# Kernel tuning notes

Measured on AMD Instinct MI355X. Metric: run time of the kernel, lower is better.

## Reference

```python
import jax, jax.numpy as jnp
import numpy as np

B = 2048; SQ = 64; PC = 24; F = 16; H = 128; D = 256; T = 128; A = 4672
NSQ = B * SQ; NPC = B * PC


def setup_inputs() -> dict:
    key = jax.random.key(0)
    ks = iter(jax.random.split(key, 48))
    def nrm(shape, s=0.05):
        return jax.random.normal(next(ks), shape, dtype=jnp.float32) * s
    def edges(e_per, src_per, dst_per):
        # per-graph local edges: graph_offset + local node index
        g = jnp.repeat(jnp.arange(B), e_per)
        src = g * src_per + jax.random.randint(next(ks), (B * e_per,), 0, src_per)
        dst = g * dst_per + jax.random.randint(next(ks), (B * e_per,), 0, dst_per)
        return jnp.stack([src, dst]).astype(jnp.int32)
    gp = jnp.repeat(jnp.arange(B), PC)
    occ_src = jnp.arange(NPC, dtype=jnp.int32)                       # each piece occupies one square
    occ_dst = (gp * SQ + jax.random.randint(next(ks), (NPC,), 0, SQ)).astype(jnp.int32)
    ei_occ = jnp.stack([occ_src, occ_dst])                           # piece -> square
    ei_rev = ei_occ[::-1]                                            # square -> piece (rev_occupied_by)
    return dict(
        x_sq=jax.random.normal(next(ks), (NSQ, F), dtype=jnp.float32),
        x_pc=jax.random.normal(next(ks), (NPC, F), dtype=jnp.float32),
        W_in_sq=nrm((F, H)), b_in_sq=jnp.zeros((H,), jnp.float32),
        W_in_pc=nrm((F, H)), b_in_pc=jnp.zeros((H,), jnp.float32),
        W_adj=nrm((H, H)), W_occ=nrm((H, H)), W_att=nrm((H, H)), W_def=nrm((H, H)), W_rev=nrm((H, H)),
        W_out=nrm((H, D)), b_out=jnp.zeros((D,), jnp.float32),
        W_pt=nrm((D, T)), b_pt=jnp.zeros((T,), jnp.float32),
        W_vt=nrm((D, T)), b_vt=jnp.zeros((T,), jnp.float32),
        W_ph=nrm((T, A)), b_ph=jnp.zeros((A,), jnp.float32),
        W_vh=nrm((T, 1)), b_vh=jnp.zeros((1,), jnp.float32),
        ei_adj=edges(420, SQ, SQ),
        ei_occ=ei_occ,
        ei_att=edges(40, PC, PC),
        ei_def=edges(40, PC, PC),
        ei_rev=ei_rev,
        square_batch=jnp.repeat(jnp.arange(B), SQ).astype(jnp.int32),
        piece_batch=gp.astype(jnp.int32),
    )


def reference(x_sq, x_pc, W_in_sq, b_in_sq, W_in_pc, b_in_pc,
              W_adj, W_occ, W_att, W_def, W_rev, W_out, b_out,
              W_pt, b_pt, W_vt, b_vt, W_ph, b_ph, W_vh, b_vh,
              ei_adj, ei_occ, ei_att, ei_def, ei_rev, square_batch, piece_batch):
    gelu = jax.nn.gelu
    seg = jax.ops.segment_sum
    # per-node-type input encoders
    h_sq = gelu(x_sq @ W_in_sq + b_in_sq)          # [NSQ, H]
    h_pc = gelu(x_pc @ W_in_pc + b_in_pc)          # [NPC, H]
    # heterogeneous message passing: gather -> linear -> scatter-sum per edge type
    agg_sq = seg(h_sq[ei_adj[0]] @ W_adj, ei_adj[1], NSQ)
    agg_sq = agg_sq + seg(h_pc[ei_occ[0]] @ W_occ, ei_occ[1], NSQ)
    agg_pc = seg(h_pc[ei_att[0]] @ W_att, ei_att[1], NPC)
    agg_pc = agg_pc + seg(h_pc[ei_def[0]] @ W_def, ei_def[1], NPC)
    agg_pc = agg_pc + seg(h_sq[ei_rev[0]] @ W_rev, ei_rev[1], NPC)
    h_sq2 = gelu(h_sq + agg_sq)
    h_pc2 = gelu(h_pc + agg_pc)
    # project to embed_dim and mean-pool per graph
    out_sq = gelu(h_sq2 @ W_out + b_out)           # [NSQ, D]
    out_pc = gelu(h_pc2 @ W_out + b_out)           # [NPC, D]
    shared = seg(out_sq, square_batch, B) / SQ + seg(out_pc, piece_batch, B) / PC  # [B, D]
    # dual trunks + heads (exactly as in ChessNetwork.forward)
    policy_logits = gelu(shared @ W_pt + b_pt) @ W_ph + b_ph        # [B, 4672]
    value = jnp.tanh(gelu(shared @ W_vt + b_vt) @ W_vh + b_vh)      # [B, 1]
    return policy_logits, value
```

## Files before the change

kernel.cpp:

```cpp
#include <hip/hip_runtime.h>

#define BATCH 2048
#define SQN 64
#define PCN 24
#define FEAT 16
#define HID 128
#define DOUT 256
#define TDIM 128
#define ADIM 4672
#define NSQT (BATCH*SQN)
#define NPCT (BATCH*PCN)
#define E_ADJ 420
#define E_ATT 40
#define E_ADJ_TOT (BATCH*E_ADJ)
#define E_ATT_TOT (BATCH*E_ATT)

typedef unsigned short u16;
typedef unsigned int u32;
typedef __attribute__((ext_vector_type(8))) short bf16x8;
typedef __attribute__((ext_vector_type(8))) unsigned short u16x8;
typedef __attribute__((ext_vector_type(4))) float f32x4;

#define OFF_WADJ_H 0
#define OFF_WADJ_L 16384
#define OFF_WOCC_H 32768
#define OFF_WOCC_L 49152
#define OFF_WATT_H 65536
#define OFF_WATT_L 81920
#define OFF_WDEF_H 98304
#define OFF_WDEF_L 114688
#define OFF_WREV_H 131072
#define OFF_WREV_L 147456
#define OFF_WOUT_H 163840
#define OFF_WOUT_L 196608
#define OFF_WPH_H  229376
#define OFF_WPH_L  827392
#define OFF_WINSQ_H 1425408
#define OFF_WINSQ_L 1429504
#define OFF_WINPC_H 1433600
#define OFF_WINPC_L 1437696
#define WB_TOTAL    1441792

#define HS_OFF   0
#define AH_OFF   32768
#define AL_OFF   49152
#define HP_OFF   65536
#define EPK_OFF  71680
#define SRT_OFF  73360
#define RSA_OFF  75040
#define CURA_OFF 75300
#define CNTA_OFF 75556
#define RSO_OFF  75812
#define CURO_OFF 76072
#define CNTO_OFF 76328
#define SRTO_OFF 76584
#define OPK_OFF  76680
#define KSQ_SMEM 76776

#define PHP_OFF  0
#define PAH_OFF  24576
#define PAL_OFF  36864
#define PEA_OFF  49152
#define PED_OFF  49472
#define PSA_OFF  49792
#define PSD_OFF  50112
#define PRSA_OFF 50432
#define PCUA_OFF 50692
#define PCNA_OFF 50948
#define PRSD_OFF 51204
#define PCUD_OFF 51464
#define PCND_OFF 51720
#define PRVS_OFF 51976
#define PRVD_OFF 52168

__device__ __forceinline__ float gelu_f(float x) {
    float z = 0.7978845608028654f * (x + 0.044715f * x * x * x);
    float e = __expf(2.0f * z);
    float t = 1.0f - 2.0f / (e + 1.0f);
    return 0.5f * x * (1.0f + t);
}
__device__ __forceinline__ u16 f2b(float x) {
    u32 u = __float_as_uint(x);
    u += 0x7fffu + ((u >> 16) & 1u);
    return (u16)(u >> 16);
}
__device__ __forceinline__ float b2f(u16 h) { return __uint_as_float(((u32)h) << 16); }
__device__ __forceinline__ void split2(float x, u16& h, u16& l) {
    u16 hh = f2b(x); h = hh; l = f2b(x - b2f(hh));
}
__device__ __forceinline__ f32x4 MFMA(bf16x8 a, bf16x8 b, f32x4 c) {
    return __builtin_amdgcn_mfma_f32_16x16x32_bf16(a, b, c, 0, 0, 0);
}
__device__ __forceinline__ bf16x8 bzero() {
    bf16x8 v = {0,0,0,0,0,0,0,0}; return v;
}
__device__ __forceinline__ void xfrag(const float* __restrict__ xrow, int g,
                                      bf16x8& ah, bf16x8& al)
{
    f32x4 a = *(const f32x4*)(xrow + g*8);
    f32x4 b = *(const f32x4*)(xrow + g*8 + 4);
    #pragma unroll
    for (int j = 0; j < 4; ++j) {
        u16 h, l;
        split2(a[j], h, l); ah[j]   = (short)h; al[j]   = (short)l;
        split2(b[j], h, l); ah[4+j] = (short)h; al[4+j] = (short)l;
    }
}

template<int NT, int RT>
__device__ __forceinline__ void gemm_nt(
    const unsigned char* Ah, const unsigned char* Al,
    const u16* __restrict__ wh, const u16* __restrict__ wl,
    int ntBase, int lane, int g, int lr, f32x4 (&c)[NT][RT])
{
    const int sw = lr << 4;
    #pragma unroll
    for (int ks = 0; ks < 4; ++ks) {
        const int ko = ks*64 + g*16;
        bf16x8 ah[RT], al[RT];
        #pragma unroll
        for (int rt = 0; rt < RT; ++rt) {
            const int ro = (rt*16 + lr)*256 + (ko ^ sw);
            ah[rt] = *(const bf16x8*)(Ah + ro);
            al[rt] = *(const bf16x8*)(Al + ro);
        }
        #pragma unroll
        for (int ntl = 0; ntl < NT; ++ntl) {
            bf16x8 bh = *(const bf16x8*)(wh + (((ntBase+ntl)*4 + ks)*64 + lane)*8);
            bf16x8 bl = *(const bf16x8*)(wl + (((ntBase+ntl)*4 + ks)*64 + lane)*8);
            #pragma unroll
            for (int rt = 0; rt < RT; ++rt) {
                c[ntl][rt] = MFMA(ah[rt], bh, c[ntl][rt]);
                c[ntl][rt] = MFMA(al[rt], bh, c[ntl][rt]);
                c[ntl][rt] = MFMA(ah[rt], bl, c[ntl][rt]);
            }
        }
    }
}

__device__ __forceinline__ void gather_f32_8(
    const unsigned char* H, const int* srt, int st, int en, int cq8, float (&acc)[16])
{
    for (int i = st; i < en; ++i) {
        const int s = srt[i];
        const unsigned char* rp = H + s*512;
        const int sw2 = (s & 15) << 4;
        #pragma unroll
        for (int u = 0; u < 4; ++u) {
            f32x4 v = *(const f32x4*)(rp + ((cq8*64 + u*16) ^ sw2));
            acc[u*4+0] += v[0]; acc[u*4+1] += v[1];
            acc[u*4+2] += v[2]; acc[u*4+3] += v[3];
        }
    }
}
__device__ __forceinline__ void gather_b16_8(
    const unsigned char* H, const int* srt, int st, int en, int cq8, float (&acc)[16])
{
    for (int i = st; i < en; ++i) {
        const int s = srt[i];
        const unsigned char* rp = H + s*256;
        const int sw2 = (s & 15) << 4;
        #pragma unroll
        for (int u = 0; u < 2; ++u) {
            u16x8 v = *(const u16x8*)(rp + ((cq8*32 + u*16) ^ sw2));
            #pragma unroll
            for (int j = 0; j < 8; ++j) acc[u*8+j] += b2f(v[j]);
        }
    }
}
__device__ __forceinline__ void writeA_8(
    unsigned char* Ah, unsigned char* Al, int d, int cq8, const float (&acc)[16])
{
    unsigned char* wh = Ah + d*256;
    unsigned char* wl = Al + d*256;
    const int dw = (d & 15) << 4;
    #pragma unroll
    for (int u = 0; u < 2; ++u) {
        u16x8 oh, ol;
        #pragma unroll
        for (int j = 0; j < 8; ++j) {
            float x = acc[u*8+j];
            u16 h = f2b(x); oh[j] = h; ol[j] = f2b(x - b2f(h));
        }
        *(u16x8*)(wh + ((cq8*32 + u*16) ^ dw)) = oh;
        *(u16x8*)(wl + ((cq8*32 + u*16) ^ dw)) = ol;
    }
}

__global__ __launch_bounds__(256) void k_prep(
    const float* __restrict__ W_adj, const float* __restrict__ W_occ,
    const float* __restrict__ W_att, const float* __restrict__ W_def,
    const float* __restrict__ W_rev, const float* __restrict__ W_out,
    const float* __restrict__ W_ph,
    const float* __restrict__ W_in_sq, const float* __restrict__ W_in_pc,
    u16* __restrict__ wb)
{
    int gid = blockIdx.x*256 + threadIdx.x;
    int fid = gid >> 6, lane = gid & 63;
    int g8 = (lane >> 4) * 8, lr = lane & 15;
    u16x8 vh, vl;
    if (fid >= 1392) {
        int f = fid - 1392;
        const float* src = (f < 8) ? W_in_sq : W_in_pc;
        int oh = (f < 8) ? OFF_WINSQ_H : OFF_WINPC_H;
        int ol = (f < 8) ? OFF_WINSQ_L : OFF_WINPC_L;
        int nt = f & 7;
        int col = nt*16 + lr;
        #pragma unroll
        for (int j = 0; j < 8; ++j) {
            int k = g8 + j;
            float v = (k < 16) ? src[k*HID + col] : 0.f;
            u16 h, l; split2(v, h, l);
            vh[j] = h; vl[j] = l;
        }
        *(u16x8*)(wb + oh + (nt*64 + lane)*8) = vh;
        *(u16x8*)(wb + ol + (nt*64 + lane)*8) = vl;
        return;
    }
    const float* src; int ld, f, oh, ol;
    if (fid < 32)       { src = W_adj; ld = HID;  f = fid;      oh = OFF_WADJ_H; ol = OFF_WADJ_L; }
    else if (fid < 64)  { src = W_occ; ld = HID;  f = fid-32;   oh = OFF_WOCC_H; ol = OFF_WOCC_L; }
    else if (fid < 96)  { src = W_att; ld = HID;  f = fid-64;   oh = OFF_WATT_H; ol = OFF_WATT_L; }
    else if (fid < 128) { src = W_def; ld = HID;  f = fid-96;   oh = OFF_WDEF_H; ol = OFF_WDEF_L; }
    else if (fid < 160) { src = W_rev; ld = HID;  f = fid-128;  oh = OFF_WREV_H; ol = OFF_WREV_L; }
    else if (fid < 224) { src = W_out; ld = DOUT; f = fid-160;  oh = OFF_WOUT_H; ol = OFF_WOUT_L; }
    else                { src = W_ph;  ld = ADIM; f = fid-224;  oh = OFF_WPH_H;  ol = OFF_WPH_L; }
    int nt = f >> 2, kb = f & 3;
    int col = nt*16 + lr;
    #pragma unroll
    for (int j = 0; j < 8; ++j) {
        int k = kb*32 + g8 + j;
        u16 h, l; split2(src[k*ld + col], h, l);
        vh[j] = h; vl[j] = l;
    }
    *(u16x8*)(wb + oh + (f*64 + lane)*8) = vh;
    *(u16x8*)(wb + ol + (f*64 + lane)*8) = vl;
}

__device__ __forceinline__ void sq_path(
    unsigned char* SMb, int b, int t,
    const float* __restrict__ x_sq, const float* __restrict__ x_pc,
    const float* __restrict__ b_in_sq, const float* __restrict__ b_in_pc,
    const float* __restrict__ b_out,
    const int* __restrict__ ei_adj, const int* __restrict__ ei_occ,
    const u16* __restrict__ wb, float* __restrict__ shared_sq)
{
    unsigned char* Hs = SMb + HS_OFF;
    unsigned char* Ah = SMb + AH_OFF;
    unsigned char* Al = SMb + AL_OFF;
    unsigned char* Hp = SMb + HP_OFF;
    int* e_pk  = (int*)(SMb + EPK_OFF);
    int* srt_a = (int*)(SMb + SRT_OFF);
    int* rs_a  = (int*)(SMb + RSA_OFF);
    int* cur_a = (int*)(SMb + CURA_OFF);
    int* cnt_a = (int*)(SMb + CNTA_OFF);
    int* rs_o  = (int*)(SMb + RSO_OFF);
    int* cur_o = (int*)(SMb + CURO_OFF);
    int* cnt_o = (int*)(SMb + CNTO_OFF);
    int* srt_o = (int*)(SMb + SRTO_OFF);
    int* o_pk  = (int*)(SMb + OPK_OFF);

    const int w = t >> 6, lane = t & 63, g = lane >> 4, lr = lane & 15;

    for (int i = t; i < E_ADJ; i += 512) {
        int s = ei_adj[b*E_ADJ + i] - b*SQN;
        int d = ei_adj[E_ADJ_TOT + b*E_ADJ + i] - b*SQN;
        e_pk[i] = s | (d << 16);
    }
    if (t < PCN) {
        int s = ei_occ[b*PCN + t] - b*PCN;
        int d = ei_occ[NPCT + b*PCN + t] - b*SQN;
        o_pk[t] = s | (d << 16);
    }
    if (t < 64) { cnt_a[t] = 0; cnt_o[t] = 0; }
    __syncthreads();

    for (int i = t; i < E_ADJ; i += 512) atomicAdd(&cnt_a[e_pk[i] >> 16], 1);
    if (t < PCN) atomicAdd(&cnt_o[o_pk[t] >> 16], 1);
    __syncthreads();

    if (t < 64) {
        int v = cnt_a[t], o0 = v;
        for (int o = 1; o < 64; o <<= 1) { int u = __shfl_up(v, o); if (t >= o) v += u; }
        rs_a[t+1] = v; cur_a[t] = v - o0; if (t == 0) rs_a[0] = 0;
    } else if (t < 128) {
        int l = t - 64;
        int v = cnt_o[l], o0 = v;
        for (int o = 1; o < 64; o <<= 1) { int u = __shfl_up(v, o); if (l >= o) v += u; }
        rs_o[l+1] = v; cur_o[l] = v - o0; if (l == 0) rs_o[0] = 0;
    }
    __syncthreads();

    for (int i = t; i < E_ADJ; i += 512) {
        int pk = e_pk[i];
        int p = atomicAdd(&cur_a[pk >> 16], 1);
        srt_a[p] = pk & 0xffff;
    }
    if (t < PCN) {
        int pk = o_pk[t];
        int p = atomicAdd(&cur_o[pk >> 16], 1);
        srt_o[p] = pk & 0xffff;
    }
    {
        const int colp = w*16 + lr;
        f32x4 ch[4];
        const f32x4 z = {0.f,0.f,0.f,0.f};
        #pragma unroll
        for (int rt = 0; rt < 4; ++rt) ch[rt] = z;
        {
            bf16x8 bh = *(const bf16x8*)(wb + OFF_WINSQ_H + (w*64 + lane)*8);
            bf16x8 bl = *(const bf16x8*)(wb + OFF_WINSQ_L + (w*64 + lane)*8);
            #pragma unroll
            for (int rt = 0; rt < 4; ++rt) {
                bf16x8 ah = bzero(), al = bzero();
                if (g < 2) xfrag(x_sq + (b*SQN + rt*16 + lr)*FEAT, g, ah, al);
                ch[rt] = MFMA(ah, bh, ch[rt]);
                ch[rt] = MFMA(al, bh, ch[rt]);
                ch[rt] = MFMA(ah, bl, ch[rt]);
            }
        }
        const float bbs = b_in_sq[colp];
        #pragma unroll
        for (int rt = 0; rt < 4; ++rt)
            #pragma unroll
            for (int r = 0; r < 4; ++r) {
                const int row = rt*16 + g*4 + r;
                float h = gelu_f(ch[rt][r] + bbs);
                *(float*)(Hs + row*512 + ((colp*4) ^ ((row&15)<<4))) = h;
            }
        f32x4 cp[2];
        cp[0] = z; cp[1] = z;
        {
            bf16x8 bh = *(const bf16x8*)(wb + OFF_WINPC_H + (w*64 + lane)*8);
            bf16x8 bl = *(const bf16x8*)(wb + OFF_WINPC_L + (w*64 + lane)*8);
            #pragma unroll
            for (int rt = 0; rt < 2; ++rt) {
                const int row = rt*16 + lr;
                bf16x8 ah = bzero(), al = bzero();
                if (g < 2 && row < PCN) xfrag(x_pc + (b*PCN + row)*FEAT, g, ah, al);
                cp[rt] = MFMA(ah, bh, cp[rt]);
                cp[rt] = MFMA(al, bh, cp[rt]);
                cp[rt] = MFMA(ah, bl, cp[rt]);
            }
        }
        const float bbp = b_in_pc[colp];
        #pragma unroll
        for (int rt = 0; rt < 2; ++rt)
            #pragma unroll
            for (int r = 0; r < 4; ++r) {
                const int row = rt*16 + g*4 + r;
                if (row < PCN) {
                    float h = gelu_f(cp[rt][r] + bbp);
                    *(u16*)(Hp + row*256 + ((colp*2) ^ ((row&15)<<4))) = f2b(h);
                }
            }
    }
    __syncthreads();

    {
        const int d = t >> 3, cq8 = t & 7;
        float acc[16];
        #pragma unroll
        for (int i = 0; i < 16; ++i) acc[i] = 0.f;
        gather_f32_8(Hs, srt_a, rs_a[d], rs_a[d+1], cq8, acc);
        writeA_8(Ah, Al, d, cq8, acc);
    }
    __syncthreads();

    f32x4 c1[1][4];
    {
        const f32x4 z = {0.f,0.f,0.f,0.f};
        #pragma unroll
        for (int rt = 0; rt < 4; ++rt) c1[0][rt] = z;
    }
    gemm_nt<1,4>(Ah, Al, wb + OFF_WADJ_H, wb + OFF_WADJ_L, w, lane, g, lr, c1);
    __syncthreads();

    {
        const int d = t >> 3, cq8 = t & 7;
        float acc[16];
        #pragma unroll
        for (int i = 0; i < 16; ++i) acc[i] = 0.f;
        gather_b16_8(Hp, srt_o, rs_o[d], rs_o[d+1], cq8, acc);
        writeA_8(Ah, Al, d, cq8, acc);
    }
    __syncthreads();

    gemm_nt<1,4>(Ah, Al, wb + OFF_WOCC_H, wb + OFF_WOCC_L, w, lane, g, lr, c1);
    __syncthreads();

    {
        const int colp = w*16 + lr;
        #pragma unroll
        for (int rt = 0; rt < 4; ++rt)
            #pragma unroll
            for (int r = 0; r < 4; ++r) {
                const int row = rt*16 + g*4 + r;
                float hv = *(const float*)(Hs + row*512 + ((colp*4) ^ ((row&15)<<4)));
                float h2 = gelu_f(c1[0][rt][r] + hv);
                u16 hh, ll; split2(h2, hh, ll);
                const int bo = row*256 + ((colp*2) ^ ((row&15)<<4));
                *(u16*)(Ah + bo) = hh;
                *(u16*)(Al + bo) = ll;
            }
    }
    __syncthreads();

    f32x4 c2[2][4];
    {
        const f32x4 z = {0.f,0.f,0.f,0.f};
        #pragma unroll
        for (int n = 0; n < 2; ++n)
            #pragma unroll
            for (int rt = 0; rt < 4; ++rt) c2[n][rt] = z;
    }
    gemm_nt<2,4>(Ah, Al, wb + OFF_WOUT_H, wb + OFF_WOUT_L, w*2, lane, g, lr, c2);
    #pragma unroll
    for (int ntl = 0; ntl < 2; ++ntl) {
        const int col = (w*2 + ntl)*16 + lr;
        const float bias = b_out[col];
        float cs = 0.f;
        #pragma unroll
        for (int rt = 0; rt < 4; ++rt)
            #pragma unroll
            for (int r = 0; r < 4; ++r) cs += gelu_f(c2[ntl][rt][r] + bias);
        cs += __shfl_xor(cs, 16);
        cs += __shfl_xor(cs, 32);
        if (lane < 16) shared_sq[b*DOUT + col] = cs * (1.0f/64.0f);
    }
}

__device__ __forceinline__ void pc_path(
    unsigned char* SMb, int pcb, int t,
    const float* __restrict__ x_sq, const float* __restrict__ x_pc,
    const float* __restrict__ b_in_sq, const float* __restrict__ b_in_pc,
    const float* __restrict__ b_out,
    const int* __restrict__ ei_att, const int* __restrict__ ei_def,
    const int* __restrict__ ei_rev,
    const u16* __restrict__ wb, float* __restrict__ shared_pc)
{
    unsigned char* Hp = SMb + PHP_OFF;
    unsigned char* Ah = SMb + PAH_OFF;
    unsigned char* Al = SMb + PAL_OFF;
    int* ea_pk = (int*)(SMb + PEA_OFF);
    int* ed_pk = (int*)(SMb + PED_OFF);
    int* srt_a = (int*)(SMb + PSA_OFF);
    int* srt_d = (int*)(SMb + PSD_OFF);
    int* rs_a  = (int*)(SMb + PRSA_OFF);
    int* cur_a = (int*)(SMb + PCUA_OFF);
    int* cnt_a = (int*)(SMb + PCNA_OFF);
    int* rs_d  = (int*)(SMb + PRSD_OFF);
    int* cur_d = (int*)(SMb + PCUD_OFF);
    int* cnt_d = (int*)(SMb + PCND_OFF);
    int* rv_s  = (int*)(SMb + PRVS_OFF);
    int* rv_d  = (int*)(SMb + PRVD_OFF);

    const int w = t >> 6, lane = t & 63, g = lane >> 4, lr = lane & 15;
    const int NR = 2*PCN;

    for (int i = t; i < 2*E_ATT; i += 512) {
        int sb = (i >= E_ATT) ? 1 : 0;
        int e = i - sb*E_ATT;
        int gb = pcb*2 + sb;
        int ro = sb*PCN - gb*PCN;
        int s = ei_att[gb*E_ATT + e] + ro;
        int d = ei_att[E_ATT_TOT + gb*E_ATT + e] + ro;
        ea_pk[i] = s | (d << 16);
        s = ei_def[gb*E_ATT + e] + ro;
        d = ei_def[E_ATT_TOT + gb*E_ATT + e] + ro;
        ed_pk[i] = s | (d << 16);
    }
    if (t < NR) {
        int sb = (t >= PCN) ? 1 : 0;
        int gb = pcb*2 + sb;
        int p = t - sb*PCN;
        rv_s[t] = ei_rev[gb*PCN + p];
        rv_d[t] = ei_rev[NPCT + gb*PCN + p] - gb*PCN + sb*PCN;
    }
    if (t < 64) { cnt_a[t] = 0; cnt_d[t] = 0; }
    __syncthreads();

    for (int i = t; i < 2*E_ATT; i += 512) {
        atomicAdd(&cnt_a[ea_pk[i] >> 16], 1);
        atomicAdd(&cnt_d[ed_pk[i] >> 16], 1);
    }
    __syncthreads();

    if (t < 64) {
        int v = cnt_a[t], o0 = v;
        for (int o = 1; o < 64; o <<= 1) { int u = __shfl_up(v, o); if (t >= o) v += u; }
        rs_a[t+1] = v; cur_a[t] = v - o0; if (t == 0) rs_a[0] = 0;
    } else if (t < 128) {
        int l = t - 64;
        int v = cnt_d[l], o0 = v;
        for (int o = 1; o < 64; o <<= 1) { int u = __shfl_up(v, o); if (l >= o) v += u; }
        rs_d[l+1] = v; cur_d[l] = v - o0; if (l == 0) rs_d[0] = 0;
    }
    __syncthreads();

    for (int i = t; i < 2*E_ATT; i += 512) {
        int pk = ea_pk[i];
        int p = atomicAdd(&cur_a[pk >> 16], 1); srt_a[p] = pk & 0xffff;
        pk = ed_pk[i];
        p = atomicAdd(&cur_d[pk >> 16], 1); srt_d[p] = pk & 0xffff;
    }
    {
        const int colp = w*16 + lr;
        const f32x4 z = {0.f,0.f,0.f,0.f};
        f32x4 cp[3];
        #pragma unroll
        for (int rt = 0; rt < 3; ++rt) cp[rt] = z;
        {
            bf16x8 bh = *(const bf16x8*)(wb + OFF_WINPC_H + (w*64 + lane)*8);
            bf16x8 bl = *(const bf16x8*)(wb + OFF_WINPC_L + (w*64 + lane)*8);
            #pragma unroll
            for (int rt = 0; rt < 3; ++rt) {
                bf16x8 ah = bzero(), al = bzero();
                if (g < 2) xfrag(x_pc + (pcb*NR + rt*16 + lr)*FEAT, g, ah, al);
                cp[rt] = MFMA(ah, bh, cp[rt]);
                cp[rt] = MFMA(al, bh, cp[rt]);
                cp[rt] = MFMA(ah, bl, cp[rt]);
            }
        }
        const float bbp = b_in_pc[colp];
        #pragma unroll
        for (int rt = 0; rt < 3; ++rt)
            #pragma unroll
            for (int r = 0; r < 4; ++r) {
                const int row = rt*16 + g*4 + r;
                float h = gelu_f(cp[rt][r] + bbp);
                *(float*)(Hp + row*512 + ((colp*4) ^ ((row&15)<<4))) = h;
            }
        f32x4 cr[3];
        #pragma unroll
        for (int rt = 0; rt < 3; ++rt) cr[rt] = z;
        {
            bf16x8 bh = *(const bf16x8*)(wb + OFF_WINSQ_H + (w*64 + lane)*8);
            bf16x8 bl = *(const bf16x8*)(wb + OFF_WINSQ_L + (w*64 + lane)*8);
            #pragma unroll
            for (int rt = 0; rt < 3; ++rt) {
                bf16x8 ah = bzero(), al = bzero();
                if (g < 2) {
                    int gr = rv_s[rt*16 + lr];
                    xfrag(x_sq + gr*FEAT, g, ah, al);
                }
                cr[rt] = MFMA(ah, bh, cr[rt]);
                cr[rt] = MFMA(al, bh, cr[rt]);
                cr[rt] = MFMA(ah, bl, cr[rt]);
            }
        }
        const float bbs = b_in_sq[colp];
        #pragma unroll
        for (int rt = 0; rt < 3; ++rt)
            #pragma unroll
            for (int r = 0; r < 4; ++r) {
                const int row0 = rt*16 + g*4 + r;
                const int dr = rv_d[row0];
                float h = gelu_f(cr[rt][r] + bbs);
                u16 hh, ll; split2(h, hh, ll);
                const int bo = dr*256 + ((colp*2) ^ ((dr&15)<<4));
                *(u16*)(Ah + bo) = hh;
                *(u16*)(Al + bo) = ll;
            }
    }
    __syncthreads();

    f32x4 c1[1][3];
    {
        const f32x4 z = {0.f,0.f,0.f,0.f};
        #pragma unroll
        for (int rt = 0; rt < 3; ++rt) c1[0][rt] = z;
    }
    gemm_nt<1,3>(Ah, Al, wb + OFF_WREV_H, wb + OFF_WREV_L, w, lane, g, lr, c1);
    __syncthreads();

    {
        const int d = t >> 3, cq8 = t & 7;
        if (d < NR) {
            float acc[16];
            #pragma unroll
            for (int i = 0; i < 16; ++i) acc[i] = 0.f;
            gather_f32_8(Hp, srt_a, rs_a[d], rs_a[d+1], cq8, acc);
            writeA_8(Ah, Al, d, cq8, acc);
        }
    }
    __syncthreads();

    gemm_nt<1,3>(Ah, Al, wb + OFF_WATT_H, wb + OFF_WATT_L, w, lane, g, lr, c1);
    __syncthreads();

    {
        const int d = t >> 3, cq8 = t & 7;
        if (d < NR) {
            float acc[16];
            #pragma unroll
            for (int i = 0; i < 16; ++i) acc[i] = 0.f;
            gather_f32_8(Hp, srt_d, rs_d[d], rs_d[d+1], cq8, acc);
            writeA_8(Ah, Al, d, cq8, acc);
        }
    }
    __syncthreads();

    gemm_nt<1,3>(Ah, Al, wb + OFF_WDEF_H, wb + OFF_WDEF_L, w, lane, g, lr, c1);
    __syncthreads();

    {
        const int colp = w*16 + lr;
        #pragma unroll
        for (int rt = 0; rt < 3; ++rt)
            #pragma unroll
            for (int r = 0; r < 4; ++r) {
                const int row = rt*16 + g*4 + r;
                float hv = *(const float*)(Hp + row*512 + ((colp*4) ^ ((row&15)<<4)));
                float h2 = gelu_f(c1[0][rt][r] + hv);
                u16 hh, ll; split2(h2, hh, ll);
                const int bo = row*256 + ((colp*2) ^ ((row&15)<<4));
                *(u16*)(Ah + bo) = hh;
                *(u16*)(Al + bo) = ll;
            }
    }
    __syncthreads();

    f32x4 c2[2][3];
    {
        const f32x4 z = {0.f,0.f,0.f,0.f};
        #pragma unroll
        for (int n = 0; n < 2; ++n)
            #pragma unroll
            for (int rt = 0; rt < 3; ++rt) c2[n][rt] = z;
    }
    gemm_nt<2,3>(Ah, Al, wb + OFF_WOUT_H, wb + OFF_WOUT_L, w*2, lane, g, lr, c2);
    #pragma unroll
    for (int ntl = 0; ntl < 2; ++ntl) {
        const int col = (w*2 + ntl)*16 + lr;
        const float bias = b_out[col];
        float s0 = 0.f, s1 = 0.f;
        #pragma unroll
        for (int r = 0; r < 4; ++r) s0 += gelu_f(c2[ntl][0][r] + bias);
        {
            float tt = 0.f;
            #pragma unroll
            for (int r = 0; r < 4; ++r) tt += gelu_f(c2[ntl][1][r] + bias);
            s0 += (g < 2) ? tt : 0.f;
            s1 += (g < 2) ? 0.f : tt;
        }
        #pragma unroll
        for (int r = 0; r < 4; ++r) s1 += gelu_f(c2[ntl][2][r] + bias);
        s0 += __shfl_xor(s0, 16); s0 += __shfl_xor(s0, 32);
        s1 += __shfl_xor(s1, 16); s1 += __shfl_xor(s1, 32);
        if (lane < 16) {
            const int b0 = pcb*2, b1 = b0 + 1;
            shared_pc[b0*DOUT + col] = s0 * (1.0f/PCN);
            shared_pc[b1*DOUT + col] = s1 * (1.0f/PCN);
        }
    }
}

__global__ __launch_bounds__(512, 4) void k_main(
    const float* __restrict__ x_sq, const float* __restrict__ x_pc,
    const float* __restrict__ b_in_sq, const float* __restrict__ b_in_pc,
    const float* __restrict__ b_out,
    const int* __restrict__ ei_adj, const int* __restrict__ ei_occ,
    const int* __restrict__ ei_att, const int* __restrict__ ei_def,
    const int* __restrict__ ei_rev,
    const u16* __restrict__ wb,
    float* __restrict__ shared_sq, float* __restrict__ shared_pc)
{
    extern __shared__ __align__(16) unsigned char SMb[];
    const int bid = blockIdx.x;
    const int grp = bid / 3, rem = bid - grp*3;
    if (rem < 2) {
        sq_path(SMb, grp*2 + rem, threadIdx.x, x_sq, x_pc, b_in_sq, b_in_pc,
                b_out, ei_adj, ei_occ, wb, shared_sq);
    } else {
        pc_path(SMb, grp, threadIdx.x, x_sq, x_pc, b_in_sq, b_in_pc,
                b_out, ei_att, ei_def, ei_rev, wb, shared_pc);
    }
}

__global__ __launch_bounds__(256) void k_head(
    const float* __restrict__ shared_sq, const float* __restrict__ shared_pc,
    const float* __restrict__ W_pt, const float* __restrict__ b_pt,
    const float* __restrict__ W_vt, const float* __restrict__ b_vt,
    const float* __restrict__ W_vh, const float* __restrict__ b_vh,
    u16* __restrict__ tpol_h, u16* __restrict__ tpol_l, float* __restrict__ out_value)
{
    __shared__ float sh[2*DOUT];
    __shared__ float vred[2*TDIM];
    const int t = threadIdx.x;
    const int hh = t >> 7, j = t & 127;
    const int b = blockIdx.x*2 + hh;
    for (int i = t; i < 2*DOUT; i += 256)
        sh[i] = shared_sq[blockIdx.x*2*DOUT + i] + shared_pc[blockIdx.x*2*DOUT + i];
    __syncthreads();
    const float* s = sh + hh*DOUT;
    float ap = b_pt[j], av = b_vt[j];
    #pragma unroll 8
    for (int k = 0; k < DOUT; ++k) {
        float sv = s[k];
        ap += sv * W_pt[k*TDIM + j];
        av += sv * W_vt[k*TDIM + j];
    }
    float tv = gelu_f(ap);
    u16 th, tl; split2(tv, th, tl);
    tpol_h[b*TDIM + j] = th;
    tpol_l[b*TDIM + j] = tl;
    vred[hh*TDIM + j] = gelu_f(av) * W_vh[j];
    __syncthreads();
    for (int stp = 64; stp > 0; stp >>= 1) {
        if (j < stp) vred[hh*TDIM + j] += vred[hh*TDIM + j + stp];
        __syncthreads();
    }
    if (j == 0) out_value[b] = tanhf(vred[hh*TDIM] + b_vh[0]);
}

__global__ __launch_bounds__(256) void k_pol(
    const u16* __restrict__ tpol_h, const u16* __restrict__ tpol_l,
    const u16* __restrict__ wb, const float* __restrict__ b_ph,
    float* __restrict__ pol)
{
    const u16* wph_h = wb + OFF_WPH_H;
    const u16* wph_l = wb + OFF_WPH_L;
    const int t = threadIdx.x, w = t >> 6, lane = t & 63, g = lane >> 4, lr = lane & 15;
    const int nt = blockIdx.x*4 + w;
    const int rbase = blockIdx.y*64;
    f32x4 acc[4];
    const f32x4 z = {0.f,0.f,0.f,0.f};
    #pragma unroll
    for (int rt = 0; rt < 4; ++rt) acc[rt] = z;
    #pragma unroll
    for (int ks = 0; ks < 4; ++ks) {
        bf16x8 bh = *(const bf16x8*)(wph_h + ((nt*4 + ks)*64 + lane)*8);
        bf16x8 bl = *(const bf16x8*)(wph_l + ((nt*4 + ks)*64 + lane)*8);
        #pragma unroll
        for (int rt = 0; rt < 4; ++rt) {
            const int ro = (rbase + rt*16 + lr)*TDIM + ks*32 + g*8;
            bf16x8 ah = *(const bf16x8*)(tpol_h + ro);
            bf16x8 al = *(const bf16x8*)(tpol_l + ro);
            acc[rt] = MFMA(ah, bh, acc[rt]);
            acc[rt] = MFMA(al, bh, acc[rt]);
            acc[rt] = MFMA(ah, bl, acc[rt]);
        }
    }
    const float bias = b_ph[nt*16 + lr];
    #pragma unroll
    for (int rt = 0; rt < 4; ++rt)
        #pragma unroll
        for (int r = 0; r < 4; ++r) {
            int row = rbase + rt*16 + g*4 + r;
            pol[(size_t)row*ADIM + nt*16 + lr] = acc[rt][r] + bias;
        }
}

extern "C" void kernel_launch(void* const* d_in, const int* in_sizes, int n_in,
                              void* d_out, int out_size, void* d_ws, size_t ws_size,
                              hipStream_t stream) {
    (void)in_sizes; (void)n_in; (void)out_size; (void)ws_size;
    const float* x_sq    = (const float*)d_in[0];
    const float* x_pc    = (const float*)d_in[1];
    const float* W_in_sq = (const float*)d_in[2];
    const float* b_in_sq = (const float*)d_in[3];
    const float* W_in_pc = (const float*)d_in[4];
    const float* b_in_pc = (const float*)d_in[5];
    const float* W_adj   = (const float*)d_in[6];
    const float* W_occ   = (const float*)d_in[7];
    const float* W_att   = (const float*)d_in[8];
    const float* W_def   = (const float*)d_in[9];
    const float* W_rev   = (const float*)d_in[10];
    const float* W_out   = (const float*)d_in[11];
    const float* b_out   = (const float*)d_in[12];
    const float* W_pt    = (const float*)d_in[13];
    const float* b_pt    = (const float*)d_in[14];
    const float* W_vt    = (const float*)d_in[15];
    const float* b_vt    = (const float*)d_in[16];
    const float* W_ph    = (const float*)d_in[17];
    const float* b_ph    = (const float*)d_in[18];
    const float* W_vh    = (const float*)d_in[19];
    const float* b_vh    = (const float*)d_in[20];
    const int* ei_adj    = (const int*)d_in[21];
    const int* ei_occ    = (const int*)d_in[22];
    const int* ei_att    = (const int*)d_in[23];
    const int* ei_def    = (const int*)d_in[24];
    const int* ei_rev    = (const int*)d_in[25];

    float* out = (float*)d_out;
    float* pol = out;
    float* val = out + (size_t)BATCH * ADIM;

    float* shared_sq = (float*)d_ws;
    float* shared_pc = shared_sq + BATCH*DOUT;
    u16* tpol_h = (u16*)(shared_pc + BATCH*DOUT);
    u16* tpol_l = tpol_h + BATCH*TDIM;
    u16* wb     = tpol_l + BATCH*TDIM;

    hipFuncSetAttribute((const void*)k_main,
                        hipFuncAttributeMaxDynamicSharedMemorySize, KSQ_SMEM);

    k_prep<<<352, 256, 0, stream>>>(W_adj, W_occ, W_att, W_def, W_rev, W_out, W_ph,
                                    W_in_sq, W_in_pc, wb);
    k_main<<<3072, 512, KSQ_SMEM, stream>>>(x_sq, x_pc, b_in_sq, b_in_pc, b_out,
                                            ei_adj, ei_occ, ei_att, ei_def, ei_rev,
                                            wb, shared_sq, shared_pc);
    k_head<<<BATCH/2, 256, 0, stream>>>(shared_sq, shared_pc, W_pt, b_pt, W_vt, b_vt,
                                        W_vh, b_vh, tpol_h, tpol_l, val);
    k_pol<<<dim3(ADIM/64, BATCH/64), 256, 0, stream>>>(tpol_h, tpol_l, wb, b_ph, pol);
}
```

Baseline: 226.8 us.

## Replace square-path CSR gather with dense adjacency-matrix MFMA and reorder linear before aggregation

The square path no longer sorts edges into CSR and gathers rows. It builds a dense 64x64 edge-count matrix and a 64x24 occupancy matrix in shared memory, multiplies H by W_adj and W_occ first, then aggregates with MFMA against those matrices. GELU is rewritten into a cheaper algebraic form, and bf16 splitting now uses the packed v_cvt_pk_bf16_f32 instruction. Edge counts stored as bf16 are exact only while they stay small, and shared memory use grows to 80 KB, which may reduce occupancy.

```diff
diff --git a/kernel.cpp b/kernel.cpp
--- a/kernel.cpp
+++ b/kernel.cpp
@@ -20,6 +20,8 @@
 typedef __attribute__((ext_vector_type(8))) short bf16x8;
 typedef __attribute__((ext_vector_type(8))) unsigned short u16x8;
 typedef __attribute__((ext_vector_type(4))) float f32x4;
+typedef __attribute__((ext_vector_type(2))) unsigned int u32x2;
+typedef __attribute__((ext_vector_type(4))) unsigned int u32x4;
 
 #define OFF_WADJ_H 0
 #define OFF_WADJ_L 16384
@@ -41,21 +43,7 @@
 #define OFF_WINPC_L 1437696
 #define WB_TOTAL    1441792
 
-#define HS_OFF   0
-#define AH_OFF   32768
-#define AL_OFF   49152
-#define HP_OFF   65536
-#define EPK_OFF  71680
-#define SRT_OFF  73360
-#define RSA_OFF  75040
-#define CURA_OFF 75300
-#define CNTA_OFF 75556
-#define RSO_OFF  75812
-#define CURO_OFF 76072
-#define CNTO_OFF 76328
-#define SRTO_OFF 76584
-#define OPK_OFF  76680
-#define KSQ_SMEM 76776
+#define K_SMEM 81920
 
 #define PHP_OFF  0
 #define PAH_OFF  24576
@@ -73,20 +61,30 @@
 #define PRVS_OFF 51976
 #define PRVD_OFF 52168
 
-__device__ __forceinline__ float gelu_f(float x) {
-    float z = 0.7978845608028654f * (x + 0.044715f * x * x * x);
-    float e = __expf(2.0f * z);
-    float t = 1.0f - 2.0f / (e + 1.0f);
-    return 0.5f * x * (1.0f + t);
-}
-__device__ __forceinline__ u16 f2b(float x) {
-    u32 u = __float_as_uint(x);
-    u += 0x7fffu + ((u >> 16) & 1u);
-    return (u16)(u >> 16);
-}
+__device__ __forceinline__ u32 cvtpk(float a, float b) {
+    u32 r;
+    asm("v_cvt_pk_bf16_f32 %0, %1, %2" : "=v"(r) : "v"(a), "v"(b));
+    return r;
+}
+__device__ __forceinline__ u16 f2b(float x) { return (u16)cvtpk(x, x); }
 __device__ __forceinline__ float b2f(u16 h) { return __uint_as_float(((u32)h) << 16); }
 __device__ __forceinline__ void split2(float x, u16& h, u16& l) {
-    u16 hh = f2b(x); h = hh; l = f2b(x - b2f(hh));
+    u32 wp = cvtpk(x, x);
+    h = (u16)wp;
+    float r = x - __uint_as_float(wp << 16);
+    l = (u16)cvtpk(r, r);
+}
+__device__ __forceinline__ void split_pk(float a, float b, u32& wh, u32& wl) {
+    wh = cvtpk(a, b);
+    float ra = a - __uint_as_float(wh << 16);
+    float rb = b - __uint_as_float(wh & 0xffff0000u);
+    wl = cvtpk(ra, rb);
+}
+__device__ __forceinline__ float gelu_f(float x) {
+    float x2 = x * x;
+    float z2 = x * __builtin_fmaf(x2, 0.0713548162f, 1.5957691216f);
+    float e = __expf(z2);
+    return x - x * __fdividef(1.0f, e + 1.0f);
 }
 __device__ __forceinline__ f32x4 MFMA(bf16x8 a, bf16x8 b, f32x4 c) {
     return __builtin_amdgcn_mfma_f32_16x16x32_bf16(a, b, c, 0, 0, 0);
@@ -97,14 +95,17 @@
 __device__ __forceinline__ void xfrag(const float* __restrict__ xrow, int g,
                                       bf16x8& ah, bf16x8& al)
 {
-    f32x4 a = *(const f32x4*)(xrow + g*8);
-    f32x4 b = *(const f32x4*)(xrow + g*8 + 4);
-    #pragma unroll
-    for (int j = 0; j < 4; ++j) {
-        u16 h, l;
-        split2(a[j], h, l); ah[j]   = (short)h; al[j]   = (short)l;
-        split2(b[j], h, l); ah[4+j] = (short)h; al[4+j] = (short)l;
-    }
+    const f32x4 a = *(const f32x4*)(xrow + g*8);
+    const f32x4 b = *(const f32x4*)(xrow + g*8 + 4);
+    u32 h0,h1,h2,h3,l0,l1,l2,l3;
+    split_pk(a[0], a[1], h0, l0);
+    split_pk(a[2], a[3], h1, l1);
+    split_pk(b[0], b[1], h2, l2);
+    split_pk(b[2], b[3], h3, l3);
+    u32x4 vh = {h0,h1,h2,h3};
+    u32x4 vl = {l0,l1,l2,l3};
+    ah = *(bf16x8*)&vh;
+    al = *(bf16x8*)&vl;
 }
 
 template<int NT, int RT>
@@ -153,21 +154,6 @@
         }
     }
 }
-__device__ __forceinline__ void gather_b16_8(
-    const unsigned char* H, const int* srt, int st, int en, int cq8, float (&acc)[16])
-{
-    for (int i = st; i < en; ++i) {
-        const int s = srt[i];
-        const unsigned char* rp = H + s*256;
-        const int sw2 = (s & 15) << 4;
-        #pragma unroll
-        for (int u = 0; u < 2; ++u) {
-            u16x8 v = *(const u16x8*)(rp + ((cq8*32 + u*16) ^ sw2));
-            #pragma unroll
-            for (int j = 0; j < 8; ++j) acc[u*8+j] += b2f(v[j]);
-        }
-    }
-}
 __device__ __forceinline__ void writeA_8(
     unsigned char* Ah, unsigned char* Al, int d, int cq8, const float (&acc)[16])
 {
@@ -176,14 +162,14 @@
     const int dw = (d & 15) << 4;
     #pragma unroll
     for (int u = 0; u < 2; ++u) {
-        u16x8 oh, ol;
-        #pragma unroll
-        for (int j = 0; j < 8; ++j) {
-            float x = acc[u*8+j];
-            u16 h = f2b(x); oh[j] = h; ol[j] = f2b(x - b2f(h));
-        }
-        *(u16x8*)(wh + ((cq8*32 + u*16) ^ dw)) = oh;
-        *(u16x8*)(wl + ((cq8*32 + u*16) ^ dw)) = ol;
+        u32 oh[4], ol[4];
+        #pragma unroll
+        for (int j = 0; j < 4; ++j)
+            split_pk(acc[u*8 + j*2], acc[u*8 + j*2 + 1], oh[j], ol[j]);
+        u32x4 vh = {oh[0], oh[1], oh[2], oh[3]};
+        u32x4 vl = {ol[0], ol[1], ol[2], ol[3]};
+        *(u32x4*)(wh + ((cq8*32 + u*16) ^ dw)) = vh;
+        *(u32x4*)(wl + ((cq8*32 + u*16) ^ dw)) = vl;
     }
 }
 
@@ -245,68 +231,51 @@
     const int* __restrict__ ei_adj, const int* __restrict__ ei_occ,
     const u16* __restrict__ wb, float* __restrict__ shared_sq)
 {
-    unsigned char* Hs = SMb + HS_OFF;
-    unsigned char* Ah = SMb + AH_OFF;
-    unsigned char* Al = SMb + AL_OFF;
-    unsigned char* Hp = SMb + HP_OFF;
-    int* e_pk  = (int*)(SMb + EPK_OFF);
-    int* srt_a = (int*)(SMb + SRT_OFF);
-    int* rs_a  = (int*)(SMb + RSA_OFF);
-    int* cur_a = (int*)(SMb + CURA_OFF);
-    int* cnt_a = (int*)(SMb + CNTA_OFF);
-    int* rs_o  = (int*)(SMb + RSO_OFF);
-    int* cur_o = (int*)(SMb + CURO_OFF);
-    int* cnt_o = (int*)(SMb + CNTO_OFF);
-    int* srt_o = (int*)(SMb + SRTO_OFF);
-    int* o_pk  = (int*)(SMb + OPK_OFF);
+    unsigned char* Hs_h  = SMb;
+    unsigned char* Hs_l  = SMb + 16384;
+    int*           Mint  = (int*)(SMb + 32768);
+    unsigned char* HOT_h = SMb + 32768;
+    unsigned char* HOT_l = SMb + 40960;
+    unsigned char* Mocc  = SMb + 49152;
+    unsigned char* A_h   = SMb + 32768;
+    unsigned char* A_l   = SMb + 49152;
+    unsigned char* Madj  = SMb + 65536;
+    unsigned char* Hp    = SMb + 73728;
 
     const int w = t >> 6, lane = t & 63, g = lane >> 4, lr = lane & 15;
+    const int colp = w*16 + lr;
+
+    #pragma unroll
+    for (int i = 0; i < 8; ++i) Mint[t + i*512] = 0;
+    ((u32*)Mocc)[t] = 0;
+    ((u32*)Mocc)[t + 512] = 0;
+    ((u32*)(Hp + 6144))[t] = 0;
+    __syncthreads();
 
     for (int i = t; i < E_ADJ; i += 512) {
         int s = ei_adj[b*E_ADJ + i] - b*SQN;
         int d = ei_adj[E_ADJ_TOT + b*E_ADJ + i] - b*SQN;
-        e_pk[i] = s | (d << 16);
+        atomicAdd(&Mint[d*64 + s], 1);
     }
     if (t < PCN) {
-        int s = ei_occ[b*PCN + t] - b*PCN;
+        int p = ei_occ[b*PCN + t] - b*PCN;
         int d = ei_occ[NPCT + b*PCN + t] - b*SQN;
-        o_pk[t] = s | (d << 16);
-    }
-    if (t < 64) { cnt_a[t] = 0; cnt_o[t] = 0; }
-    __syncthreads();
-
-    for (int i = t; i < E_ADJ; i += 512) atomicAdd(&cnt_a[e_pk[i] >> 16], 1);
-    if (t < PCN) atomicAdd(&cnt_o[o_pk[t] >> 16], 1);
-    __syncthreads();
-
-    if (t < 64) {
-        int v = cnt_a[t], o0 = v;
-        for (int o = 1; o < 64; o <<= 1) { int u = __shfl_up(v, o); if (t >= o) v += u; }
-        rs_a[t+1] = v; cur_a[t] = v - o0; if (t == 0) rs_a[0] = 0;
-    } else if (t < 128) {
-        int l = t - 64;
-        int v = cnt_o[l], o0 = v;
-        for (int o = 1; o < 64; o <<= 1) { int u = __shfl_up(v, o); if (l >= o) v += u; }
-        rs_o[l+1] = v; cur_o[l] = v - o0; if (l == 0) rs_o[0] = 0;
-    }
-    __syncthreads();
-
-    for (int i = t; i < E_ADJ; i += 512) {
-        int pk = e_pk[i];
-        int p = atomicAdd(&cur_a[pk >> 16], 1);
-        srt_a[p] = pk & 0xffff;
-    }
-    if (t < PCN) {
-        int pk = o_pk[t];
-        int p = atomicAdd(&cur_o[pk >> 16], 1);
-        srt_o[p] = pk & 0xffff;
-    }
-    {
-        const int colp = w*16 + lr;
-        f32x4 ch[4];
+        *(u16*)(Mocc + d*64 + ((p*2) ^ ((d&3)<<4))) = 0x3F80;
+    }
+    __syncthreads();
+
+    #pragma unroll
+    for (int ii = 0; ii < 4; ++ii) {
+        int i = t + ii*512;
+        int row = i >> 5, cp = i & 31;
+        float v0 = (float)Mint[row*64 + cp*2];
+        float v1 = (float)Mint[row*64 + cp*2 + 1];
+        *(u32*)(Madj + row*128 + ((cp*4) ^ ((row&7)<<4))) = cvtpk(v0, v1);
+    }
+    float hv[16];
+    {
         const f32x4 z = {0.f,0.f,0.f,0.f};
-        #pragma unroll
-        for (int rt = 0; rt < 4; ++rt) ch[rt] = z;
+        f32x4 ch[4] = {z,z,z,z};
         {
             bf16x8 bh = *(const bf16x8*)(wb + OFF_WINSQ_H + (w*64 + lane)*8);
             bf16x8 bl = *(const bf16x8*)(wb + OFF_WINSQ_L + (w*64 + lane)*8);
@@ -326,10 +295,13 @@
             for (int r = 0; r < 4; ++r) {
                 const int row = rt*16 + g*4 + r;
                 float h = gelu_f(ch[rt][r] + bbs);
-                *(float*)(Hs + row*512 + ((colp*4) ^ ((row&15)<<4))) = h;
-            }
-        f32x4 cp[2];
-        cp[0] = z; cp[1] = z;
+                hv[rt*4 + r] = h;
+                u16 hh, ll; split2(h, hh, ll);
+                const int bo = row*256 + ((colp*2) ^ ((row&15)<<4));
+                *(u16*)(Hs_h + bo) = hh;
+                *(u16*)(Hs_l + bo) = ll;
+            }
+        f32x4 cp2[2] = {z, z};
         {
             bf16x8 bh = *(const bf16x8*)(wb + OFF_WINPC_H + (w*64 + lane)*8);
             bf16x8 bl = *(const bf16x8*)(wb + OFF_WINPC_L + (w*64 + lane)*8);
@@ -338,9 +310,9 @@
                 const int row = rt*16 + lr;
                 bf16x8 ah = bzero(), al = bzero();
                 if (g < 2 && row < PCN) xfrag(x_pc + (b*PCN + row)*FEAT, g, ah, al);
-                cp[rt] = MFMA(ah, bh, cp[rt]);
-                cp[rt] = MFMA(al, bh, cp[rt]);
-                cp[rt] = MFMA(ah, bl, cp[rt]);
+                cp2[rt] = MFMA(ah, bh, cp2[rt]);
+                cp2[rt] = MFMA(al, bh, cp2[rt]);
+                cp2[rt] = MFMA(ah, bl, cp2[rt]);
             }
         }
         const float bbp = b_in_pc[colp];
@@ -350,60 +322,114 @@
             for (int r = 0; r < 4; ++r) {
                 const int row = rt*16 + g*4 + r;
                 if (row < PCN) {
-                    float h = gelu_f(cp[rt][r] + bbp);
+                    float h = gelu_f(cp2[rt][r] + bbp);
                     *(u16*)(Hp + row*256 + ((colp*2) ^ ((row&15)<<4))) = f2b(h);
                 }
             }
     }
     __syncthreads();
 
-    {
-        const int d = t >> 3, cq8 = t & 7;
-        float acc[16];
-        #pragma unroll
-        for (int i = 0; i < 16; ++i) acc[i] = 0.f;
-        gather_f32_8(Hs, srt_a, rs_a[d], rs_a[d+1], cq8, acc);
-        writeA_8(Ah, Al, d, cq8, acc);
-    }
-    __syncthreads();
-
-    f32x4 c1[1][4];
+    f32x4 hwj[4], hwo[2];
     {
         const f32x4 z = {0.f,0.f,0.f,0.f};
-        #pragma unroll
-        for (int rt = 0; rt < 4; ++rt) c1[0][rt] = z;
-    }
-    gemm_nt<1,4>(Ah, Al, wb + OFF_WADJ_H, wb + OFF_WADJ_L, w, lane, g, lr, c1);
-    __syncthreads();
-
-    {
-        const int d = t >> 3, cq8 = t & 7;
-        float acc[16];
-        #pragma unroll
-        for (int i = 0; i < 16; ++i) acc[i] = 0.f;
-        gather_b16_8(Hp, srt_o, rs_o[d], rs_o[d+1], cq8, acc);
-        writeA_8(Ah, Al, d, cq8, acc);
-    }
-    __syncthreads();
-
-    gemm_nt<1,4>(Ah, Al, wb + OFF_WOCC_H, wb + OFF_WOCC_L, w, lane, g, lr, c1);
-    __syncthreads();
-
-    {
-        const int colp = w*16 + lr;
-        #pragma unroll
-        for (int rt = 0; rt < 4; ++rt)
-            #pragma unroll
-            for (int r = 0; r < 4; ++r) {
-                const int row = rt*16 + g*4 + r;
-                float hv = *(const float*)(Hs + row*512 + ((colp*4) ^ ((row&15)<<4)));
-                float h2 = gelu_f(c1[0][rt][r] + hv);
-                u16 hh, ll; split2(h2, hh, ll);
-                const int bo = row*256 + ((colp*2) ^ ((row&15)<<4));
-                *(u16*)(Ah + bo) = hh;
-                *(u16*)(Al + bo) = ll;
-            }
-    }
+        hwj[0]=z; hwj[1]=z; hwj[2]=z; hwj[3]=z; hwo[0]=z; hwo[1]=z;
+        const int sw15 = lr << 4;
+        #pragma unroll
+        for (int ks = 0; ks < 4; ++ks) {
+            const int ko = ks*64 + g*16;
+            bf16x8 bh = *(const bf16x8*)(wb + OFF_WADJ_H + ((w*4 + ks)*64 + lane)*8);
+            bf16x8 bl = *(const bf16x8*)(wb + OFF_WADJ_L + ((w*4 + ks)*64 + lane)*8);
+            #pragma unroll
+            for (int rt = 0; rt < 4; ++rt) {
+                const int ro = (rt*16 + lr)*256 + (ko ^ sw15);
+                bf16x8 ah = *(const bf16x8*)(Hs_h + ro);
+                bf16x8 al = *(const bf16x8*)(Hs_l + ro);
+                hwj[rt] = MFMA(ah, bh, hwj[rt]);
+                hwj[rt] = MFMA(al, bh, hwj[rt]);
+                hwj[rt] = MFMA(ah, bl, hwj[rt]);
+            }
+            bf16x8 oh = *(const bf16x8*)(wb + OFF_WOCC_H + ((w*4 + ks)*64 + lane)*8);
+            bf16x8 ol = *(const bf16x8*)(wb + OFF_WOCC_L + ((w*4 + ks)*64 + lane)*8);
+            #pragma unroll
+            for (int rt = 0; rt < 2; ++rt) {
+                const int ro = (rt*16 + lr)*256 + (ko ^ sw15);
+                bf16x8 ah = *(const bf16x8*)(Hp + ro);
+                hwo[rt] = MFMA(ah, oh, hwo[rt]);
+                hwo[rt] = MFMA(ah, ol, hwo[rt]);
+            }
+        }
+    }
+    __syncthreads();
+
+    {
+        const int swj = (lr & 7) << 4;
+        #pragma unroll
+        for (int rt = 0; rt < 4; ++rt) {
+            u32 h01, l01, h23, l23;
+            split_pk(hwj[rt][0], hwj[rt][1], h01, l01);
+            split_pk(hwj[rt][2], hwj[rt][3], h23, l23);
+            const int off = colp*128 + ((rt*32 + g*8) ^ swj);
+            *(u32x2*)(Hs_h + off) = (u32x2){h01, h23};
+            *(u32x2*)(Hs_l + off) = (u32x2){l01, l23};
+        }
+        const int swo = (lr & 3) << 4;
+        #pragma unroll
+        for (int rt = 0; rt < 2; ++rt) {
+            u32 h01, l01, h23, l23;
+            split_pk(hwo[rt][0], hwo[rt][1], h01, l01);
+            split_pk(hwo[rt][2], hwo[rt][3], h23, l23);
+            const int off = colp*64 + ((rt*32 + g*8) ^ swo);
+            *(u32x2*)(HOT_h + off) = (u32x2){h01, h23};
+            *(u32x2*)(HOT_l + off) = (u32x2){l01, l23};
+        }
+    }
+    __syncthreads();
+
+    f32x4 c1[4];
+    {
+        const f32x4 z = {0.f,0.f,0.f,0.f};
+        c1[0]=z; c1[1]=z; c1[2]=z; c1[3]=z;
+        const int swj = (lr & 7) << 4;
+        #pragma unroll
+        for (int ks = 0; ks < 2; ++ks) {
+            const int bo = colp*128 + ((ks*64 + g*16) ^ swj);
+            bf16x8 bh = *(const bf16x8*)(Hs_h + bo);
+            bf16x8 bl = *(const bf16x8*)(Hs_l + bo);
+            #pragma unroll
+            for (int rt = 0; rt < 4; ++rt) {
+                const int ao = (rt*16 + lr)*128 + ((ks*64 + g*16) ^ swj);
+                bf16x8 am = *(const bf16x8*)(Madj + ao);
+                c1[rt] = MFMA(am, bh, c1[rt]);
+                c1[rt] = MFMA(am, bl, c1[rt]);
+            }
+        }
+        const int swo = (lr & 3) << 4;
+        {
+            const int bo = colp*64 + ((g*16) ^ swo);
+            bf16x8 bh = *(const bf16x8*)(HOT_h + bo);
+            bf16x8 bl = *(const bf16x8*)(HOT_l + bo);
+            #pragma unroll
+            for (int rt = 0; rt < 4; ++rt) {
+                const int ao = (rt*16 + lr)*64 + ((g*16) ^ swo);
+                bf16x8 am = *(const bf16x8*)(Mocc + ao);
+                c1[rt] = MFMA(am, bh, c1[rt]);
+                c1[rt] = MFMA(am, bl, c1[rt]);
+            }
+        }
+    }
+    __syncthreads();
+
+    #pragma unroll
+    for (int rt = 0; rt < 4; ++rt)
+        #pragma unroll
+        for (int r = 0; r < 4; ++r) {
+            const int row = rt*16 + g*4 + r;
+            float h2 = gelu_f(c1[rt][r] + hv[rt*4 + r]);
+            u16 hh, ll; split2(h2, hh, ll);
+            const int bo = row*256 + ((colp*2) ^ ((row&15)<<4));
+            *(u16*)(A_h + bo) = hh;
+            *(u16*)(A_l + bo) = ll;
+        }
     __syncthreads();
 
     f32x4 c2[2][4];
@@ -414,7 +440,7 @@
             #pragma unroll
             for (int rt = 0; rt < 4; ++rt) c2[n][rt] = z;
     }
-    gemm_nt<2,4>(Ah, Al, wb + OFF_WOUT_H, wb + OFF_WOUT_L, w*2, lane, g, lr, c2);
+    gemm_nt<2,4>(A_h, A_l, wb + OFF_WOUT_H, wb + OFF_WOUT_L, w*2, lane, g, lr, c2);
     #pragma unroll
     for (int ntl = 0; ntl < 2; ++ntl) {
         const int col = (w*2 + ntl)*16 + lr;
@@ -507,9 +533,7 @@
     {
         const int colp = w*16 + lr;
         const f32x4 z = {0.f,0.f,0.f,0.f};
-        f32x4 cp[3];
-        #pragma unroll
-        for (int rt = 0; rt < 3; ++rt) cp[rt] = z;
+        f32x4 cp[3] = {z,z,z};
         {
             bf16x8 bh = *(const bf16x8*)(wb + OFF_WINPC_H + (w*64 + lane)*8);
             bf16x8 bl = *(const bf16x8*)(wb + OFF_WINPC_L + (w*64 + lane)*8);
@@ -531,9 +555,7 @@
                 float h = gelu_f(cp[rt][r] + bbp);
                 *(float*)(Hp + row*512 + ((colp*4) ^ ((row&15)<<4))) = h;
             }
-        f32x4 cr[3];
-        #pragma unroll
-        for (int rt = 0; rt < 3; ++rt) cr[rt] = z;
+        f32x4 cr[3] = {z,z,z};
         {
             bf16x8 bh = *(const bf16x8*)(wb + OFF_WINSQ_H + (w*64 + lane)*8);
             bf16x8 bl = *(const bf16x8*)(wb + OFF_WINSQ_L + (w*64 + lane)*8);
@@ -611,8 +633,8 @@
             #pragma unroll
             for (int r = 0; r < 4; ++r) {
                 const int row = rt*16 + g*4 + r;
-                float hv = *(const float*)(Hp + row*512 + ((colp*4) ^ ((row&15)<<4)));
-                float h2 = gelu_f(c1[0][rt][r] + hv);
+                float hvv = *(const float*)(Hp + row*512 + ((colp*4) ^ ((row&15)<<4)));
+                float h2 = gelu_f(c1[0][rt][r] + hvv);
                 u16 hh, ll; split2(h2, hh, ll);
                 const int bo = row*256 + ((colp*2) ^ ((row&15)<<4));
                 *(u16*)(Ah + bo) = hh;
@@ -794,13 +816,13 @@
     u16* wb     = tpol_l + BATCH*TDIM;
 
     hipFuncSetAttribute((const void*)k_main,
-                        hipFuncAttributeMaxDynamicSharedMemorySize, KSQ_SMEM);
+                        hipFuncAttributeMaxDynamicSharedMemorySize, K_SMEM);
 
     k_prep<<<352, 256, 0, stream>>>(W_adj, W_occ, W_att, W_def, W_rev, W_out, W_ph,
                                     W_in_sq, W_in_pc, wb);
-    k_main<<<3072, 512, KSQ_SMEM, stream>>>(x_sq, x_pc, b_in_sq, b_in_pc, b_out,
-                                            ei_adj, ei_occ, ei_att, ei_def, ei_rev,
-                                            wb, shared_sq, shared_pc);
+    k_main<<<3072, 512, K_SMEM, stream>>>(x_sq, x_pc, b_in_sq, b_in_pc, b_out,
+                                          ei_adj, ei_occ, ei_att, ei_def, ei_rev,
+                                          wb, shared_sq, shared_pc);
     k_head<<<BATCH/2, 256, 0, stream>>>(shared_sq, shared_pc, W_pt, b_pt, W_vt, b_vt,
                                         W_vh, b_vh, tpol_h, tpol_l, val);
     k_pol<<<dim3(ADIM/64, BATCH/64), 256, 0, stream>>>(tpol_h, tpol_l, wb, b_ph, pol);
```

Measured after the change: 198.2 us. 12.6% less time.
